# Kernel optimization log

Measured on AMD Instinct MI355X. Metric: run time of the kernel, lower is better.

The kernel has to match this reference:

```python
import jax, jax.numpy as jnp
import numpy as np

IN_CH, OUT_CH, K, STRIDE = 128, 256, 3, 1

def setup_inputs() -> dict:
    key = jax.random.key(0)
    kx, kw = jax.random.split(key)
    x = jax.random.normal(kx, (32, IN_CH, 56, 56), dtype=jnp.float32)
    # xavier_uniform: bound = sqrt(6 / (fan_in + fan_out)), fans include receptive field
    fan_in = IN_CH * K * K
    fan_out = OUT_CH * K * K
    bound = float(np.sqrt(6.0 / (fan_in + fan_out)))
    weight = jax.random.uniform(kw, (OUT_CH, IN_CH, K, K), dtype=jnp.float32,
                                minval=-bound, maxval=bound)
    bias = jnp.zeros((OUT_CH,), dtype=jnp.float32)
    return {"x": x, "weight": weight, "bias": bias}

def reference(x, weight, bias):
    # VALID (no-padding) conv, stride STRIDE, NCHW layout, OIHW kernel
    out = jax.lax.conv_general_dilated(
        x, weight,
        window_strides=(STRIDE, STRIDE),
        padding="VALID",
        dimension_numbers=("NCHW", "OIHW", "NCHW"))
    return out + bias[None, :, None, None]
```

## Files before the change

kernel.cpp:

```cpp
#include <hip/hip_runtime.h>
#include <hip/hip_bf16.h>
#include <stdint.h>

#define NB    32
#define CIN   128
#define HIN   56
#define HW    (HIN*HIN)
#define OCH   256
#define OHW   54
#define SPB   (OHW*OHW)
#define KSZ   (CIN*9)
#define BM    256
#define BN    256
#define BK    64
#define NKS   (KSZ/BK)
#define TOTC  (NB*SPB)
#define NT    365

typedef __attribute__((ext_vector_type(8))) short bf16x8;
typedef __attribute__((ext_vector_type(4))) float f32x4;

typedef __attribute__((address_space(1))) const uint32_t g_u32;
typedef __attribute__((address_space(3))) uint32_t l_u32;
static __device__ __forceinline__ void gl_lds16(const void* g, void* l) {
    __builtin_amdgcn_global_load_lds((g_u32*)g, (l_u32*)l, 16, 0, 0);
}

__global__ void xpose_cast(const float* __restrict__ x, __hip_bfloat16* __restrict__ xt) {
    __shared__ float tile[32][33];
    const int hw0 = blockIdx.x * 32;
    const int c0  = blockIdx.y * 32;
    const int n   = blockIdx.z;
    const int tx = threadIdx.x, ty = threadIdx.y;
    const float* xp = x + ((size_t)n*CIN + c0)*HW + hw0;
    #pragma unroll
    for (int i = ty; i < 32; i += 8)
        tile[i][tx] = xp[(size_t)i*HW + tx];
    __syncthreads();
    const int t = ty*32 + tx;
    const int hwl = t >> 3, q = t & 7;
    ushort4 v;
    v.x = __bfloat16_as_ushort(__float2bfloat16(tile[q*4+0][hwl]));
    v.y = __bfloat16_as_ushort(__float2bfloat16(tile[q*4+1][hwl]));
    v.z = __bfloat16_as_ushort(__float2bfloat16(tile[q*4+2][hwl]));
    v.w = __bfloat16_as_ushort(__float2bfloat16(tile[q*4+3][hwl]));
    __hip_bfloat16* op = xt + ((size_t)n*HW + hw0 + hwl)*CIN + c0 + q*4;
    *(ushort4*)op = v;
}

__global__ void wcast(const float* __restrict__ w, __hip_bfloat16* __restrict__ wt) {
    int tid = blockIdx.x*256 + threadIdx.x;
    if (tid >= OCH*KSZ) return;
    int oc = tid / KSZ, r = tid % KSZ;
    int pos = r >> 7, ic = r & 127;
    wt[tid] = __float2bfloat16(w[((size_t)(oc*CIN + ic))*9 + pos]);
}

__global__ __launch_bounds__(512, 2)
void conv_mfma(const __hip_bfloat16* __restrict__ xt,
               const __hip_bfloat16* __restrict__ wt,
               const float* __restrict__ bias,
               float* __restrict__ out) {
    __shared__ uint4 smem[8192];

    const int t = threadIdx.x;
    const int tile = blockIdx.x;
    const int lane = t & 63, wid = t >> 6;
    const int wm = wid >> 2, wn = wid & 3;
    const int lr = lane & 15, lq = lane >> 4;

    const __hip_bfloat16* aptr[2];
    const __hip_bfloat16* bptr[2];
    #pragma unroll
    for (int i = 0; i < 2; ++i) {
        int q = i*512 + t;
        int row = q >> 2, j = q & 3;
        int ls = j ^ (row & 3);
        aptr[i] = wt + (size_t)row*KSZ + ls*8;
        int colg = tile*BN + row; if (colg >= TOTC) colg = TOTC - 1;
        int n = colg / SPB, rem = colg - n*SPB;
        int oh = rem / OHW, ow = rem - oh*OHW;
        bptr[i] = xt + ((size_t)(n*HIN + oh)*HIN + ow)*CIN + ls*8;
    }

    auto issueU = [&](int ks, int mat, int X) {
        uint4* dst = smem + (ks & 1)*4096 + mat*2048 + X*1024 + t;
        if (mat == 0) {
            const int off = ks*BK + X*32;
            gl_lds16(aptr[0] + off, dst);
            gl_lds16(aptr[1] + off, dst + 512);
        } else {
            const int pos = ks >> 1;
            const int kh = pos / 3, kw = pos - kh*3;
            const int off = (kh*HIN + kw)*CIN + (ks & 1)*64 + X*32;
            gl_lds16(bptr[0] + off, dst);
            gl_lds16(bptr[1] + off, dst + 512);
        }
    };

    f32x4 acc[8][4];
    #pragma unroll
    for (int i = 0; i < 8; ++i)
        #pragma unroll
        for (int j = 0; j < 4; ++j)
            acc[i][j] = (f32x4){0.f, 0.f, 0.f, 0.f};

    #define MFMA_BF16 __builtin_amdgcn_mfma_f32_16x16x32_bf16
    #define RD_A4(arr, MIB, KK) \
        _Pragma("unroll") \
        for (int ii = 0; ii < 4; ++ii) { \
            int ra = wm*128 + ((MIB)+ii)*16 + lr; \
            arr[ii] = *(bf16x8*)&Ab[(KK)*1024 + ra*4 + (lq ^ (ra & 3))]; \
        }
    #define RD_B4(arr, KK) \
        _Pragma("unroll") \
        for (int ni = 0; ni < 4; ++ni) { \
            int rb = wn*64 + ni*16 + lr; \
            arr[ni] = *(bf16x8*)&Bb[(KK)*1024 + rb*4 + (lq ^ (rb & 3))]; \
        }
    #define PH_OPEN() \
        __builtin_amdgcn_s_barrier(); \
        asm volatile("s_waitcnt lgkmcnt(0)"); \
        __builtin_amdgcn_sched_barrier(0);
    #define MFMA_BLK(AARR, MIB, BARR) \
        __builtin_amdgcn_s_setprio(1); \
        _Pragma("unroll") \
        for (int ii = 0; ii < 4; ++ii) \
            _Pragma("unroll") \
            for (int ni = 0; ni < 4; ++ni) \
                acc[(MIB)+ii][ni] = MFMA_BF16(AARR[ii], BARR[ni], acc[(MIB)+ii][ni], 0, 0, 0); \
        __builtin_amdgcn_s_setprio(0);

    issueU(0, 0, 0); issueU(0, 1, 0); issueU(0, 0, 1); issueU(0, 1, 1);
    asm volatile("s_waitcnt vmcnt(4)" ::: "memory");
    __builtin_amdgcn_s_barrier();
    __builtin_amdgcn_sched_barrier(0);

    for (int ks = 0; ks < NKS; ++ks) {
        const uint4* Ab = smem + (ks & 1)*4096;
        const uint4* Bb = Ab + 2048;
        const bool pf = (ks + 1 < NKS);
        bf16x8 a[4], b[4];

        RD_A4(a, 0, 0) RD_B4(b, 0)
        if (pf) issueU(ks + 1, 0, 0);
        PH_OPEN()
        MFMA_BLK(a, 0, b)
        __builtin_amdgcn_s_barrier();

        RD_A4(a, 4, 0)
        if (pf) issueU(ks + 1, 1, 0);
        PH_OPEN()
        MFMA_BLK(a, 4, b)
        if (pf) asm volatile("s_waitcnt vmcnt(4)" ::: "memory");
        else    asm volatile("s_waitcnt vmcnt(0)" ::: "memory");
        __builtin_amdgcn_s_barrier();
        __builtin_amdgcn_sched_barrier(0);

        RD_A4(a, 0, 1) RD_B4(b, 1)
        if (pf) issueU(ks + 1, 0, 1);
        PH_OPEN()
        MFMA_BLK(a, 0, b)
        __builtin_amdgcn_s_barrier();

        RD_A4(a, 4, 1)
        if (pf) issueU(ks + 1, 1, 1);
        PH_OPEN()
        MFMA_BLK(a, 4, b)
        if (pf) asm volatile("s_waitcnt vmcnt(4)" ::: "memory");
        __builtin_amdgcn_s_barrier();
        __builtin_amdgcn_sched_barrier(0);
    }

    float (*eps)[260] = (float (*)[260])smem;
    const int cl4 = (t & 63) * 4;
    const int rsub = t >> 6;
    const int colg = tile*BN + cl4;
    int nn = 0, sp = 0;
    if (colg < TOTC) { nn = colg / SPB; sp = colg - nn*SPB; }
    #pragma unroll
    for (int h = 0; h < 4; ++h) {
        if (wm == (h >> 1)) {
            const int mib = (h & 1) * 4;
            #pragma unroll
            for (int ii = 0; ii < 4; ++ii) {
                int rl = ii*16 + lq*4;
                #pragma unroll
                for (int ni = 0; ni < 4; ++ni) {
                    int cl = wn*64 + ni*16 + lr;
                    #pragma unroll
                    for (int r = 0; r < 4; ++r)
                        eps[rl + r][cl] = acc[mib + ii][ni][r];
                }
            }
        }
        __syncthreads();
        if (colg < TOTC) {
            #pragma unroll
            for (int pass = 0; pass < 8; ++pass) {
                int rl = pass*8 + rsub;
                int rg = h*64 + rl;
                f32x4 v = *(f32x4*)&eps[rl][cl4];
                v = v + bias[rg];
                *(f32x4*)&out[((size_t)nn*OCH + rg)*SPB + sp] = v;
            }
        }
        __syncthreads();
    }
}

__global__ void conv_naive(const float* __restrict__ x, const float* __restrict__ w,
                           const float* __restrict__ bias, float* __restrict__ out) {
    size_t tid = (size_t)blockIdx.x*256 + threadIdx.x;
    const size_t total = (size_t)NB*OCH*SPB;
    if (tid >= total) return;
    int col = (int)(tid % SPB);
    int oc  = (int)((tid / SPB) % OCH);
    int n   = (int)(tid / ((size_t)SPB*OCH));
    int oh = col / OHW, ow = col % OHW;
    float s = bias[oc];
    for (int ic = 0; ic < CIN; ++ic)
        #pragma unroll
        for (int kh = 0; kh < 3; ++kh)
            #pragma unroll
            for (int kw = 0; kw < 3; ++kw)
                s += x[((size_t)(n*CIN+ic)*HIN + oh+kh)*HIN + ow+kw]
                   * w[((size_t)(oc*CIN+ic)*3 + kh)*3 + kw];
    out[tid] = s;
}

extern "C" void kernel_launch(void* const* d_in, const int* in_sizes, int n_in,
                              void* d_out, int out_size, void* d_ws, size_t ws_size,
                              hipStream_t stream) {
    const float* x    = (const float*)d_in[0];
    const float* w    = (const float*)d_in[1];
    const float* bias = (const float*)d_in[2];
    float* out = (float*)d_out;

    const size_t xt_bytes = (size_t)NB*HW*CIN*sizeof(__hip_bfloat16);
    const size_t wt_bytes = (size_t)OCH*KSZ*sizeof(__hip_bfloat16);

    if (ws_size >= xt_bytes + wt_bytes) {
        __hip_bfloat16* xt  = (__hip_bfloat16*)d_ws;
        __hip_bfloat16* wtp = (__hip_bfloat16*)((char*)d_ws + xt_bytes);
        hipLaunchKernelGGL(xpose_cast, dim3(HW/32, CIN/32, NB), dim3(32, 8), 0, stream, x, xt);
        hipLaunchKernelGGL(wcast, dim3((OCH*KSZ + 255)/256), dim3(256), 0, stream, w, wtp);
        hipLaunchKernelGGL(conv_mfma, dim3(NT), dim3(512), 0, stream, xt, wtp, bias, out);
    } else {
        size_t total = (size_t)NB*OCH*SPB;
        hipLaunchKernelGGL(conv_naive, dim3((unsigned)((total + 255)/256)), dim3(256), 0, stream,
                           x, w, bias, out);
    }
}
```

Baseline: 101.1 us.

## Switch conv GEMM to BK=32 triple-buffered pipeline with XCD-aware tile remap

Halves the K-step to 32 and replaces the double-buffered, four-phase main loop with a three-stage LDS ring that prefetches two steps ahead and needs only one barrier per step. LDS fragment offsets are precomputed, and the swizzle changes to use (row>>1)&3 to reduce bank conflicts. Block indices are remapped so that each XCD processes a contiguous range of tiles, which is meant to improve L2 locality. In exchange there are twice as many loop iterations with less MFMA work per barrier, and the ring uses less LDS (96KB rather than 128KB), so the epilogue's staging buffer is worth checking.

```diff
diff --git a/kernel.cpp b/kernel.cpp
--- a/kernel.cpp
+++ b/kernel.cpp
@@ -12,7 +12,7 @@
 #define KSZ   (CIN*9)
 #define BM    256
 #define BN    256
-#define BK    64
+#define BK    32
 #define NKS   (KSZ/BK)
 #define TOTC  (NB*SPB)
 #define NT    365
@@ -61,10 +61,14 @@
                const __hip_bfloat16* __restrict__ wt,
                const float* __restrict__ bias,
                float* __restrict__ out) {
-    __shared__ uint4 smem[8192];
+    __shared__ uint4 smem[3*2048];
 
     const int t = threadIdx.x;
-    const int tile = blockIdx.x;
+    {   }
+    const int orig = blockIdx.x;
+    const int xcd = orig & 7;
+    const int tile = (xcd < 5 ? xcd*46 : 5*46 + (xcd-5)*45) + (orig >> 3);
+
     const int lane = t & 63, wid = t >> 6;
     const int wm = wid >> 2, wn = wid & 3;
     const int lr = lane & 15, lq = lane >> 4;
@@ -75,7 +79,7 @@
     for (int i = 0; i < 2; ++i) {
         int q = i*512 + t;
         int row = q >> 2, j = q & 3;
-        int ls = j ^ (row & 3);
+        int ls = j ^ ((row >> 1) & 3);
         aptr[i] = wt + (size_t)row*KSZ + ls*8;
         int colg = tile*BN + row; if (colg >= TOTC) colg = TOTC - 1;
         int n = colg / SPB, rem = colg - n*SPB;
@@ -83,20 +87,29 @@
         bptr[i] = xt + ((size_t)(n*HIN + oh)*HIN + ow)*CIN + ls*8;
     }
 
-    auto issueU = [&](int ks, int mat, int X) {
-        uint4* dst = smem + (ks & 1)*4096 + mat*2048 + X*1024 + t;
-        if (mat == 0) {
-            const int off = ks*BK + X*32;
-            gl_lds16(aptr[0] + off, dst);
-            gl_lds16(aptr[1] + off, dst + 512);
-        } else {
-            const int pos = ks >> 1;
-            const int kh = pos / 3, kw = pos - kh*3;
-            const int off = (kh*HIN + kw)*CIN + (ks & 1)*64 + X*32;
-            gl_lds16(bptr[0] + off, dst);
-            gl_lds16(bptr[1] + off, dst + 512);
-        }
+    auto issueT = [&](int ks) {
+        uint4* dst = smem + (ks % 3)*2048;
+        const int aoff = ks*BK;
+        const int pos = ks >> 2;
+        const int kh = pos / 3, kw = pos - kh*3;
+        const int boff = (kh*HIN + kw)*CIN + (ks & 3)*32;
+        gl_lds16(aptr[0] + aoff, dst + t);
+        gl_lds16(aptr[1] + aoff, dst + 512 + t);
+        gl_lds16(bptr[0] + boff, dst + 1024 + t);
+        gl_lds16(bptr[1] + boff, dst + 1536 + t);
     };
+
+    int ao[8], bo[4];
+    #pragma unroll
+    for (int mi = 0; mi < 8; ++mi) {
+        int ra = wm*128 + mi*16 + lr;
+        ao[mi] = ra*4 + (lq ^ ((ra >> 1) & 3));
+    }
+    #pragma unroll
+    for (int ni = 0; ni < 4; ++ni) {
+        int rb = wn*64 + ni*16 + lr;
+        bo[ni] = 1024 + rb*4 + (lq ^ ((rb >> 1) & 3));
+    }
 
     f32x4 acc[8][4];
     #pragma unroll
@@ -106,71 +119,52 @@
             acc[i][j] = (f32x4){0.f, 0.f, 0.f, 0.f};
 
     #define MFMA_BF16 __builtin_amdgcn_mfma_f32_16x16x32_bf16
-    #define RD_A4(arr, MIB, KK) \
-        _Pragma("unroll") \
-        for (int ii = 0; ii < 4; ++ii) { \
-            int ra = wm*128 + ((MIB)+ii)*16 + lr; \
-            arr[ii] = *(bf16x8*)&Ab[(KK)*1024 + ra*4 + (lq ^ (ra & 3))]; \
-        }
-    #define RD_B4(arr, KK) \
-        _Pragma("unroll") \
-        for (int ni = 0; ni < 4; ++ni) { \
-            int rb = wn*64 + ni*16 + lr; \
-            arr[ni] = *(bf16x8*)&Bb[(KK)*1024 + rb*4 + (lq ^ (rb & 3))]; \
-        }
-    #define PH_OPEN() \
-        __builtin_amdgcn_s_barrier(); \
-        asm volatile("s_waitcnt lgkmcnt(0)"); \
-        __builtin_amdgcn_sched_barrier(0);
-    #define MFMA_BLK(AARR, MIB, BARR) \
-        __builtin_amdgcn_s_setprio(1); \
-        _Pragma("unroll") \
-        for (int ii = 0; ii < 4; ++ii) \
-            _Pragma("unroll") \
-            for (int ni = 0; ni < 4; ++ni) \
-                acc[(MIB)+ii][ni] = MFMA_BF16(AARR[ii], BARR[ni], acc[(MIB)+ii][ni], 0, 0, 0); \
-        __builtin_amdgcn_s_setprio(0);
-
-    issueU(0, 0, 0); issueU(0, 1, 0); issueU(0, 0, 1); issueU(0, 1, 1);
+
+    issueT(0); issueT(1);
     asm volatile("s_waitcnt vmcnt(4)" ::: "memory");
     __builtin_amdgcn_s_barrier();
     __builtin_amdgcn_sched_barrier(0);
 
     for (int ks = 0; ks < NKS; ++ks) {
-        const uint4* Ab = smem + (ks & 1)*4096;
-        const uint4* Bb = Ab + 2048;
-        const bool pf = (ks + 1 < NKS);
-        bf16x8 a[4], b[4];
-
-        RD_A4(a, 0, 0) RD_B4(b, 0)
-        if (pf) issueU(ks + 1, 0, 0);
-        PH_OPEN()
-        MFMA_BLK(a, 0, b)
-        __builtin_amdgcn_s_barrier();
-
-        RD_A4(a, 4, 0)
-        if (pf) issueU(ks + 1, 1, 0);
-        PH_OPEN()
-        MFMA_BLK(a, 4, b)
-        if (pf) asm volatile("s_waitcnt vmcnt(4)" ::: "memory");
-        else    asm volatile("s_waitcnt vmcnt(0)" ::: "memory");
-        __builtin_amdgcn_s_barrier();
+        const uint4* buf = smem + (ks % 3)*2048;
+        bf16x8 a0[4], a1[4], b[4];
+        #pragma unroll
+        for (int mi = 0; mi < 4; ++mi) a0[mi] = *(bf16x8*)&buf[ao[mi]];
+        #pragma unroll
+        for (int ni = 0; ni < 4; ++ni) b[ni]  = *(bf16x8*)&buf[bo[ni]];
+        if (ks + 2 < NKS) issueT(ks + 2);
+        #pragma unroll
+        for (int mi = 0; mi < 4; ++mi) a1[mi] = *(bf16x8*)&buf[ao[4 + mi]];
+
+        asm volatile("s_waitcnt lgkmcnt(4)" ::: "memory");
         __builtin_amdgcn_sched_barrier(0);
-
-        RD_A4(a, 0, 1) RD_B4(b, 1)
-        if (pf) issueU(ks + 1, 0, 1);
-        PH_OPEN()
-        MFMA_BLK(a, 0, b)
-        __builtin_amdgcn_s_barrier();
-
-        RD_A4(a, 4, 1)
-        if (pf) issueU(ks + 1, 1, 1);
-        PH_OPEN()
-        MFMA_BLK(a, 4, b)
-        if (pf) asm volatile("s_waitcnt vmcnt(4)" ::: "memory");
-        __builtin_amdgcn_s_barrier();
+        __builtin_amdgcn_s_setprio(1);
+        #pragma unroll
+        for (int mi = 0; mi < 4; ++mi)
+            #pragma unroll
+            for (int ni = 0; ni < 4; ++ni)
+                acc[mi][ni] = MFMA_BF16(a0[mi], b[ni], acc[mi][ni], 0, 0, 0);
+        __builtin_amdgcn_s_setprio(0);
+
+        asm volatile("s_waitcnt lgkmcnt(0)" ::: "memory");
         __builtin_amdgcn_sched_barrier(0);
-    }
+        __builtin_amdgcn_s_setprio(1);
+        #pragma unroll
+        for (int mi = 0; mi < 4; ++mi)
+            #pragma unroll
+            for (int ni = 0; ni < 4; ++ni)
+                acc[4+mi][ni] = MFMA_BF16(a1[mi], b[ni], acc[4+mi][ni], 0, 0, 0);
+        __builtin_amdgcn_s_setprio(0);
+
+        if (ks + 1 < NKS) {
+            if (ks + 2 < NKS) asm volatile("s_waitcnt vmcnt(4)" ::: "memory");
+            else              asm volatile("s_waitcnt vmcnt(0)" ::: "memory");
+            __builtin_amdgcn_s_barrier();
+            __builtin_amdgcn_sched_barrier(0);
+        }
+    }
+
+    __syncthreads();
 
     float (*eps)[260] = (float (*)[260])smem;
     const int cl4 = (t & 63) * 4;
```

Result: faster. 94.64 us (-6.4%).
